# Kernel optimization log

Hardware: AMD Instinct MI355X
Metric: run time of the kernel (lower is better)

## Reference

```python
import jax, jax.numpy as jnp
import numpy as np

TEMPERATURE = 0.07
EPS = 1e-12  # matches torch F.normalize default eps


def setup_inputs() -> dict:
    key = jax.random.key(0)
    k1, k2 = jax.random.split(key)
    B, D = 8192, 256
    anchor = jax.random.normal(k1, (B, D), dtype=jnp.float32)
    positive = jax.random.normal(k2, (B, D), dtype=jnp.float32)
    return {"anchor": anchor, "positive": positive}


def _l2_normalize(x):
    # torch F.normalize(p=2, dim=1): x / max(||x||, eps)
    n = jnp.sqrt(jnp.sum(x * x, axis=1, keepdims=True))
    return x / jnp.maximum(n, EPS)


def reference(anchor, positive):
    a = _l2_normalize(anchor)
    p = _l2_normalize(positive)
    # normalized vectors -> cosine similarity is just a GEMM: (B, B)
    sim = jnp.einsum('id,jd->ij', a, p)
    B = sim.shape[0]
    # hard negative mining: max over off-diagonal entries per row
    neg = jnp.where(jnp.eye(B, dtype=bool), -jnp.inf, sim)
    max_neg = jnp.max(neg, axis=-1)  # (B,)
    logits = jnp.concatenate([sim, max_neg[:, None]], axis=1) / TEMPERATURE  # (B, B+1)
    labels = jnp.arange(B)
    logp = jax.nn.log_softmax(logits, axis=-1)
    loss = -jnp.mean(jnp.take_along_axis(logp, labels[:, None], axis=1))
    return loss
```

## Files before the change

### kernel.cpp

```cpp
#include <hip/hip_runtime.h>
#include <hip/hip_bf16.h>

using floatx4 = __attribute__((ext_vector_type(4))) float;
using int4v   = __attribute__((ext_vector_type(4))) int;
using int8v   = __attribute__((ext_vector_type(8))) int;

#define TEMP_INV 14.285714285714286f
#define DD 256
#define BM 128
#define NCT 8
#define SC1 127

typedef const __attribute__((address_space(1))) unsigned int* gptr_t;
typedef __attribute__((address_space(3))) unsigned int* lptr_t;

__device__ __forceinline__ void async_cp16(const void* g, void* l) {
  __builtin_amdgcn_global_load_lds((gptr_t)g, (lptr_t)l, 16, 0, 0);
}

__global__ __launch_bounds__(256) void nrm_kernel(
    const float* __restrict__ anchor, const float* __restrict__ positive,
    unsigned char* __restrict__ a8, unsigned char* __restrict__ p8,
    float* __restrict__ diag, float* __restrict__ out) {
  if (blockIdx.x == 0 && threadIdx.x == 0) out[0] = 0.f;
  const int wave = threadIdx.x >> 6;
  const int lane = threadIdx.x & 63;
  const int row  = blockIdx.x * 4 + wave;
  const float4 va = ((const float4*)(anchor   + (size_t)row * DD))[lane];
  const float4 vp = ((const float4*)(positive + (size_t)row * DD))[lane];
  float sa = va.x * va.x + va.y * va.y + va.z * va.z + va.w * va.w;
  float sp = vp.x * vp.x + vp.y * vp.y + vp.z * vp.z + vp.w * vp.w;
#pragma unroll
  for (int m = 32; m >= 1; m >>= 1) {
    sa += __shfl_xor(sa, m, 64);
    sp += __shfl_xor(sp, m, 64);
  }
  const float ka = 1.0f / fmaxf(sqrtf(sa), 1e-12f);
  const float kp = 1.0f / fmaxf(sqrtf(sp), 1e-12f);
  int pa = __builtin_amdgcn_cvt_pk_fp8_f32(va.x * ka, va.y * ka, 0, false);
  pa     = __builtin_amdgcn_cvt_pk_fp8_f32(va.z * ka, va.w * ka, pa, true);
  int pp = __builtin_amdgcn_cvt_pk_fp8_f32(vp.x * kp, vp.y * kp, 0, false);
  pp     = __builtin_amdgcn_cvt_pk_fp8_f32(vp.z * kp, vp.w * kp, pp, true);
  ((int*)(a8 + (size_t)row * DD))[lane] = pa;
  ((int*)(p8 + (size_t)row * DD))[lane] = pp;
  float d = __builtin_amdgcn_cvt_f32_fp8(pa, 0) * __builtin_amdgcn_cvt_f32_fp8(pp, 0)
          + __builtin_amdgcn_cvt_f32_fp8(pa, 1) * __builtin_amdgcn_cvt_f32_fp8(pp, 1)
          + __builtin_amdgcn_cvt_f32_fp8(pa, 2) * __builtin_amdgcn_cvt_f32_fp8(pp, 2)
          + __builtin_amdgcn_cvt_f32_fp8(pa, 3) * __builtin_amdgcn_cvt_f32_fp8(pp, 3);
#pragma unroll
  for (int m = 32; m >= 1; m >>= 1) d += __shfl_xor(d, m, 64);
  if (lane == 0) diag[row] = d;
}

__device__ __forceinline__ int8v fragLDS(const unsigned char* S, int row, int ks,
                                         int quad, int l16) {
  const int c0 = ks * 8 + quad * 2;
  const int4v lo = *(const int4v*)(S + row * DD + (((c0 + 0) ^ l16) << 4));
  const int4v hi = *(const int4v*)(S + row * DD + (((c0 + 1) ^ l16) << 4));
  return __builtin_shufflevector(lo, hi, 0, 1, 2, 3, 4, 5, 6, 7);
}

__device__ __forceinline__ int8v fragG(const unsigned char* g) {
  const int4v lo = *(const int4v*)(g);
  const int4v hi = *(const int4v*)(g + 16);
  return __builtin_shufflevector(lo, hi, 0, 1, 2, 3, 4, 5, 6, 7);
}

__global__ __launch_bounds__(512, 4) void gemm_stats(
    const unsigned char* __restrict__ a8, const unsigned char* __restrict__ p8,
    float* __restrict__ rsum, float* __restrict__ rmax, int Btot) {
  __shared__ __align__(16) unsigned char Bs[2][BM * DD];
  __shared__ float red_sum[2][BM];
  __shared__ float red_max[2][BM];

  const int t = threadIdx.x;
  const int wave = t >> 6, lane = t & 63;
  const int wm = wave & 3, wn = wave >> 2;
  const int quad = lane >> 4, l16 = lane & 15;
  const int row0    = blockIdx.y * BM;
  const int colbase = blockIdx.x * (NCT * BM);
  const bool hasdiag = ((int)(blockIdx.y >> 3) == (int)blockIdx.x);

  const int r4 = lane >> 4;
  const int cg = lane & 15;

  int8v a_frag[2][2];
  {
    const unsigned char* ab =
        a8 + (size_t)(row0 + wm * 32 + l16) * DD + quad * 32;
#pragma unroll
    for (int mi = 0; mi < 2; ++mi)
#pragma unroll
      for (int ks = 0; ks < 2; ++ks)
        a_frag[mi][ks] = fragG(ab + mi * 16 * DD + ks * 128);
  }

#pragma unroll
  for (int q = 0; q < 4; ++q) {
    const int rb = q * 32 + wave * 4;
    const int r  = rb + r4;
    async_cp16(p8 + (size_t)(colbase + r) * DD + (cg ^ (r & 15)) * 16,
               &Bs[0][rb * DD]);
  }

  float se_run[2][4], mx_run[2][4];
#pragma unroll
  for (int a = 0; a < 2; ++a)
#pragma unroll
    for (int b = 0; b < 4; ++b) { se_run[a][b] = 0.f; mx_run[a][b] = -INFINITY; }

  for (int ct = 0; ct < NCT; ++ct) {
    __syncthreads();

    if (ct + 1 < NCT) {
      const int colb = colbase + (ct + 1) * BM;
      unsigned char* dst = &Bs[(ct + 1) & 1][0];
#pragma unroll
      for (int q = 0; q < 4; ++q) {
        const int rb = q * 32 + wave * 4;
        const int r  = rb + r4;
        async_cp16(p8 + (size_t)(colb + r) * DD + (cg ^ (r & 15)) * 16,
                   dst + rb * DD);
      }
    }

    floatx4 acc[2][4];
#pragma unroll
    for (int a = 0; a < 2; ++a)
#pragma unroll
      for (int b = 0; b < 4; ++b) acc[a][b] = (floatx4){0.f, 0.f, 0.f, 0.f};

    const unsigned char* Bcur = &Bs[ct & 1][0];
#pragma unroll
    for (int ks = 0; ks < 2; ++ks) {
#pragma unroll
      for (int ni = 0; ni < 4; ++ni) {
        const int8v bf = fragLDS(Bcur, wn * 64 + ni * 16 + l16, ks, quad, l16);
        acc[0][ni] = __builtin_amdgcn_mfma_scale_f32_16x16x128_f8f6f4(
            a_frag[0][ks], bf, acc[0][ni], 0, 0, 0, SC1, 0, SC1);
        acc[1][ni] = __builtin_amdgcn_mfma_scale_f32_16x16x128_f8f6f4(
            a_frag[1][ks], bf, acc[1][ni], 0, 0, 0, SC1, 0, SC1);
      }
    }

    const int col0 = colbase + ct * BM;
    if (!hasdiag) {
#pragma unroll
      for (int mi = 0; mi < 2; ++mi)
#pragma unroll
        for (int reg = 0; reg < 4; ++reg)
#pragma unroll
          for (int ni = 0; ni < 4; ++ni) {
            const float s = acc[mi][ni][reg];
            se_run[mi][reg] += __expf(s * TEMP_INV);
            mx_run[mi][reg] = fmaxf(mx_run[mi][reg], s);
          }
    } else {
#pragma unroll
      for (int mi = 0; mi < 2; ++mi)
#pragma unroll
        for (int reg = 0; reg < 4; ++reg) {
          const int i = row0 + wm * 32 + mi * 16 + quad * 4 + reg;
#pragma unroll
          for (int ni = 0; ni < 4; ++ni) {
            const float s = acc[mi][ni][reg];
            const int j = col0 + wn * 64 + ni * 16 + l16;
            se_run[mi][reg] += __expf(s * TEMP_INV);
            mx_run[mi][reg] = fmaxf(mx_run[mi][reg], (i == j) ? -INFINITY : s);
          }
        }
    }
  }

#pragma unroll
  for (int mi = 0; mi < 2; ++mi) {
#pragma unroll
    for (int reg = 0; reg < 4; ++reg) {
      float se = se_run[mi][reg], mx = mx_run[mi][reg];
#pragma unroll
      for (int m = 1; m < 16; m <<= 1) {
        se += __shfl_xor(se, m, 64);
        mx = fmaxf(mx, __shfl_xor(mx, m, 64));
      }
      if (l16 == 0) {
        const int rb = wm * 32 + mi * 16 + quad * 4 + reg;
        red_sum[wn][rb] = se;
        red_max[wn][rb] = mx;
      }
    }
  }
  __syncthreads();
  if (t < BM) {
    rsum[(size_t)blockIdx.x * Btot + row0 + t] = red_sum[0][t] + red_sum[1][t];
    rmax[(size_t)blockIdx.x * Btot + row0 + t] = fmaxf(red_max[0][t], red_max[1][t]);
  }
}

__global__ __launch_bounds__(256) void row_loss_kernel(
    const float* __restrict__ rsum, const float* __restrict__ rmax,
    const float* __restrict__ diag, float* __restrict__ out, int Btot, int NG) {
  const int i = blockIdx.x * 256 + threadIdx.x;
  float s = 0.f, m = -INFINITY;
  for (int c = 0; c < NG; ++c) {
    s += rsum[(size_t)c * Btot + i];
    m = fmaxf(m, rmax[(size_t)c * Btot + i]);
  }
  float rl = __logf(s + __expf(m * TEMP_INV)) - diag[i] * TEMP_INV;
#pragma unroll
  for (int mm = 32; mm >= 1; mm >>= 1) rl += __shfl_xor(rl, mm, 64);
  __shared__ float red[4];
  if ((threadIdx.x & 63) == 0) red[threadIdx.x >> 6] = rl;
  __syncthreads();
  if (threadIdx.x == 0)
    atomicAdd(out, (red[0] + red[1] + red[2] + red[3]) / (float)Btot);
}

extern "C" void kernel_launch(void* const* d_in, const int* in_sizes, int n_in,
                              void* d_out, int out_size, void* d_ws, size_t ws_size,
                              hipStream_t stream) {
  const float* anchor   = (const float*)d_in[0];
  const float* positive = (const float*)d_in[1];
  const int B  = in_sizes[0] / DD;
  const int NG = B / (BM * NCT);
  const size_t BD = (size_t)B * DD;

  unsigned char* a8 = (unsigned char*)d_ws;
  unsigned char* p8 = a8 + BD;
  float* rsum  = (float*)(p8 + BD);
  float* rmax  = rsum + (size_t)NG * B;
  float* diag  = rmax + (size_t)NG * B;

  nrm_kernel<<<B / 4, 256, 0, stream>>>(anchor, positive, a8, p8, diag,
                                        (float*)d_out);
  dim3 g2(NG, B / BM);
  gemm_stats<<<g2, 512, 0, stream>>>(a8, p8, rsum, rmax, B);
  row_loss_kernel<<<B / 256, 256, 0, stream>>>(rsum, rmax, diag, (float*)d_out, B, NG);
}
```

Before: 108.4 us.

## Split column tile into two phases with barrier-synchronized MFMA and epilogue interleaving

Each column tile is now processed in two halves. Every half loads its LDS B fragments, issues half of the next tile's async global-to-LDS copies, hits a block barrier, then runs its MFMAs at raised wave priority followed by the exp/max epilogue. The aim is to spread memory traffic across the tile and to stagger the MFMA and exp work between waves, in a ping-pong style, so tensor and vector units overlap. The cost is extra s_barrier calls per tile and fixed sched_barrier points, which limit how freely the compiler can schedule instructions.

```diff
diff --git a/kernel.cpp b/kernel.cpp
--- a/kernel.cpp
+++ b/kernel.cpp
@@ -66,6 +66,11 @@
   return __builtin_shufflevector(lo, hi, 0, 1, 2, 3, 4, 5, 6, 7);
 }
 
+__device__ __forceinline__ floatx4 mfma_sc(int8v a, int8v b, floatx4 c) {
+  return __builtin_amdgcn_mfma_scale_f32_16x16x128_f8f6f4(a, b, c, 0, 0, 0,
+                                                          SC1, 0, SC1);
+}
+
 __global__ __launch_bounds__(512, 4) void gemm_stats(
     const unsigned char* __restrict__ a8, const unsigned char* __restrict__ p8,
     float* __restrict__ rsum, float* __restrict__ rmax, int Btot) {
@@ -112,63 +117,78 @@
   for (int ct = 0; ct < NCT; ++ct) {
     __syncthreads();
 
-    if (ct + 1 < NCT) {
-      const int colb = colbase + (ct + 1) * BM;
-      unsigned char* dst = &Bs[(ct + 1) & 1][0];
-#pragma unroll
-      for (int q = 0; q < 4; ++q) {
-        const int rb = q * 32 + wave * 4;
-        const int r  = rb + r4;
-        async_cp16(p8 + (size_t)(colb + r) * DD + (cg ^ (r & 15)) * 16,
-                   dst + rb * DD);
-      }
-    }
-
-    floatx4 acc[2][4];
-#pragma unroll
-    for (int a = 0; a < 2; ++a)
-#pragma unroll
-      for (int b = 0; b < 4; ++b) acc[a][b] = (floatx4){0.f, 0.f, 0.f, 0.f};
-
     const unsigned char* Bcur = &Bs[ct & 1][0];
-#pragma unroll
-    for (int ks = 0; ks < 2; ++ks) {
-#pragma unroll
-      for (int ni = 0; ni < 4; ++ni) {
-        const int8v bf = fragLDS(Bcur, wn * 64 + ni * 16 + l16, ks, quad, l16);
-        acc[0][ni] = __builtin_amdgcn_mfma_scale_f32_16x16x128_f8f6f4(
-            a_frag[0][ks], bf, acc[0][ni], 0, 0, 0, SC1, 0, SC1);
-        acc[1][ni] = __builtin_amdgcn_mfma_scale_f32_16x16x128_f8f6f4(
-            a_frag[1][ks], bf, acc[1][ni], 0, 0, 0, SC1, 0, SC1);
-      }
-    }
-
+    unsigned char* Bnxt = &Bs[(ct + 1) & 1][0];
+    const int colb = colbase + (ct + 1) * BM;
+    const bool dostage = (ct + 1 < NCT);
     const int col0 = colbase + ct * BM;
-    if (!hasdiag) {
-#pragma unroll
-      for (int mi = 0; mi < 2; ++mi)
-#pragma unroll
-        for (int reg = 0; reg < 4; ++reg)
-#pragma unroll
-          for (int ni = 0; ni < 4; ++ni) {
-            const float s = acc[mi][ni][reg];
-            se_run[mi][reg] += __expf(s * TEMP_INV);
-            mx_run[mi][reg] = fmaxf(mx_run[mi][reg], s);
+
+#pragma unroll
+    for (int p = 0; p < 2; ++p) {
+      const int nA = 2 * p, nB = 2 * p + 1;
+      const int8v bfA0 = fragLDS(Bcur, wn * 64 + nA * 16 + l16, 0, quad, l16);
+      const int8v bfA1 = fragLDS(Bcur, wn * 64 + nA * 16 + l16, 1, quad, l16);
+      const int8v bfB0 = fragLDS(Bcur, wn * 64 + nB * 16 + l16, 0, quad, l16);
+      const int8v bfB1 = fragLDS(Bcur, wn * 64 + nB * 16 + l16, 1, quad, l16);
+      if (dostage) {
+#pragma unroll
+        for (int q = 2 * p; q < 2 * p + 2; ++q) {
+          const int rb = q * 32 + wave * 4;
+          const int r  = rb + r4;
+          async_cp16(p8 + (size_t)(colb + r) * DD + (cg ^ (r & 15)) * 16,
+                     Bnxt + rb * DD);
+        }
+      }
+      __builtin_amdgcn_sched_barrier(0);
+      __builtin_amdgcn_s_barrier();
+      asm volatile("s_waitcnt lgkmcnt(0)" ::: "memory");
+      __builtin_amdgcn_sched_barrier(0);
+
+      floatx4 acc[2][2];
+#pragma unroll
+      for (int a = 0; a < 2; ++a)
+#pragma unroll
+        for (int b = 0; b < 2; ++b) acc[a][b] = (floatx4){0.f, 0.f, 0.f, 0.f};
+
+      __builtin_amdgcn_s_setprio(1);
+      acc[0][0] = mfma_sc(a_frag[0][0], bfA0, acc[0][0]);
+      acc[0][0] = mfma_sc(a_frag[0][1], bfA1, acc[0][0]);
+      acc[1][0] = mfma_sc(a_frag[1][0], bfA0, acc[1][0]);
+      acc[1][0] = mfma_sc(a_frag[1][1], bfA1, acc[1][0]);
+      acc[0][1] = mfma_sc(a_frag[0][0], bfB0, acc[0][1]);
+      acc[0][1] = mfma_sc(a_frag[0][1], bfB1, acc[0][1]);
+      acc[1][1] = mfma_sc(a_frag[1][0], bfB0, acc[1][1]);
+      acc[1][1] = mfma_sc(a_frag[1][1], bfB1, acc[1][1]);
+      __builtin_amdgcn_s_setprio(0);
+      __builtin_amdgcn_sched_barrier(0);
+      __builtin_amdgcn_s_barrier();
+
+      if (!hasdiag) {
+#pragma unroll
+        for (int mi = 0; mi < 2; ++mi)
+#pragma unroll
+          for (int reg = 0; reg < 4; ++reg)
+#pragma unroll
+            for (int h = 0; h < 2; ++h) {
+              const float s = acc[mi][h][reg];
+              se_run[mi][reg] += __expf(s * TEMP_INV);
+              mx_run[mi][reg] = fmaxf(mx_run[mi][reg], s);
+            }
+      } else {
+#pragma unroll
+        for (int mi = 0; mi < 2; ++mi)
+#pragma unroll
+          for (int reg = 0; reg < 4; ++reg) {
+            const int i = row0 + wm * 32 + mi * 16 + quad * 4 + reg;
+#pragma unroll
+            for (int h = 0; h < 2; ++h) {
+              const float s = acc[mi][h][reg];
+              const int j = col0 + wn * 64 + (2 * p + h) * 16 + l16;
+              se_run[mi][reg] += __expf(s * TEMP_INV);
+              mx_run[mi][reg] = fmaxf(mx_run[mi][reg], (i == j) ? -INFINITY : s);
+            }
           }
-    } else {
-#pragma unroll
-      for (int mi = 0; mi < 2; ++mi)
-#pragma unroll
-        for (int reg = 0; reg < 4; ++reg) {
-          const int i = row0 + wm * 32 + mi * 16 + quad * 4 + reg;
-#pragma unroll
-          for (int ni = 0; ni < 4; ++ni) {
-            const float s = acc[mi][ni][reg];
-            const int j = col0 + wn * 64 + ni * 16 + l16;
-            se_run[mi][reg] += __expf(s * TEMP_INV);
-            mx_run[mi][reg] = fmaxf(mx_run[mi][reg], (i == j) ? -INFINITY : s);
-          }
-        }
+      }
     }
   }
 
```

Measured after the change: 168.6 us. 1.56x slower.

## Use 256-thread blocks with single LDS buffer and split-half compute/epilogue overlap

Applied to the files above, without the earlier changes.

The GEMM-stats kernel now runs 4 waves per block, each wave covering 32 rows across the full 128-column tile, instead of 8 waves split 4x2. The double-buffered LDS tile becomes a single buffer. The next tile's async load is issued after the second half's MFMAs, so it overlaps the second half's exp/max epilogue. Per-block column groups are halved (NCT 4, giving twice as many grid column groups), and the cross-wave LDS reduction of row stats is dropped in favour of direct global writes. This cuts LDS use and barriers, at the cost of less prefetch distance and more partial rows for the final reduction kernel to combine.

```diff
diff --git a/kernel.cpp b/kernel.cpp
--- a/kernel.cpp
+++ b/kernel.cpp
@@ -7,8 +7,9 @@
 
 #define TEMP_INV 14.285714285714286f
 #define DD 256
-#define BM 128
-#define NCT 8
+#define BMR 128
+#define BNC 128
+#define NCT 4
 #define SC1 127
 
 typedef const __attribute__((address_space(1))) unsigned int* gptr_t;
@@ -66,28 +67,26 @@
   return __builtin_shufflevector(lo, hi, 0, 1, 2, 3, 4, 5, 6, 7);
 }
 
-__global__ __launch_bounds__(512, 4) void gemm_stats(
+__device__ __forceinline__ floatx4 mfma_sc(int8v a, int8v b, floatx4 c) {
+  return __builtin_amdgcn_mfma_scale_f32_16x16x128_f8f6f4(a, b, c, 0, 0, 0,
+                                                          SC1, 0, SC1);
+}
+
+__global__ __launch_bounds__(256, 4) void gemm_stats(
     const unsigned char* __restrict__ a8, const unsigned char* __restrict__ p8,
     float* __restrict__ rsum, float* __restrict__ rmax, int Btot) {
-  __shared__ __align__(16) unsigned char Bs[2][BM * DD];
-  __shared__ float red_sum[2][BM];
-  __shared__ float red_max[2][BM];
+  __shared__ __align__(16) unsigned char Bs[BNC * DD];
 
   const int t = threadIdx.x;
   const int wave = t >> 6, lane = t & 63;
-  const int wm = wave & 3, wn = wave >> 2;
   const int quad = lane >> 4, l16 = lane & 15;
-  const int row0    = blockIdx.y * BM;
-  const int colbase = blockIdx.x * (NCT * BM);
-  const bool hasdiag = ((int)(blockIdx.y >> 3) == (int)blockIdx.x);
-
-  const int r4 = lane >> 4;
-  const int cg = lane & 15;
+  const int row0    = blockIdx.y * BMR;
+  const int colbase = blockIdx.x * (NCT * BNC);
 
   int8v a_frag[2][2];
   {
     const unsigned char* ab =
-        a8 + (size_t)(row0 + wm * 32 + l16) * DD + quad * 32;
+        a8 + (size_t)(row0 + wave * 32 + l16) * DD + quad * 32;
 #pragma unroll
     for (int mi = 0; mi < 2; ++mi)
 #pragma unroll
@@ -96,11 +95,11 @@
   }
 
 #pragma unroll
-  for (int q = 0; q < 4; ++q) {
-    const int rb = q * 32 + wave * 4;
-    const int r  = rb + r4;
-    async_cp16(p8 + (size_t)(colbase + r) * DD + (cg ^ (r & 15)) * 16,
-               &Bs[0][rb * DD]);
+  for (int q = 0; q < 8; ++q) {
+    const int rb = q * 16 + wave * 4;
+    const int r  = rb + quad;
+    async_cp16(p8 + (size_t)(colbase + r) * DD + ((l16 ^ (r & 15)) << 4),
+               &Bs[rb * DD]);
   }
 
   float se_run[2][4], mx_run[2][4];
@@ -111,39 +110,77 @@
 
   for (int ct = 0; ct < NCT; ++ct) {
     __syncthreads();
-
+    const int col0 = colbase + ct * BNC;
+    const bool hasdiag = (blockIdx.y == blockIdx.x * NCT + ct);
+
+    floatx4 acc[2][4];
+#pragma unroll
+    for (int a = 0; a < 2; ++a)
+#pragma unroll
+      for (int b = 0; b < 4; ++b) acc[a][b] = (floatx4){0.f, 0.f, 0.f, 0.f};
+#pragma unroll
+    for (int ni = 0; ni < 4; ++ni) {
+      const int8v bf0 = fragLDS(Bs, ni * 16 + l16, 0, quad, l16);
+      const int8v bf1 = fragLDS(Bs, ni * 16 + l16, 1, quad, l16);
+      acc[0][ni] = mfma_sc(a_frag[0][0], bf0, acc[0][ni]);
+      acc[0][ni] = mfma_sc(a_frag[0][1], bf1, acc[0][ni]);
+      acc[1][ni] = mfma_sc(a_frag[1][0], bf0, acc[1][ni]);
+      acc[1][ni] = mfma_sc(a_frag[1][1], bf1, acc[1][ni]);
+    }
+    if (!hasdiag) {
+#pragma unroll
+      for (int mi = 0; mi < 2; ++mi)
+#pragma unroll
+        for (int reg = 0; reg < 4; ++reg)
+#pragma unroll
+          for (int ni = 0; ni < 4; ++ni) {
+            const float s = acc[mi][ni][reg];
+            se_run[mi][reg] += __expf(s * TEMP_INV);
+            mx_run[mi][reg] = fmaxf(mx_run[mi][reg], s);
+          }
+    } else {
+#pragma unroll
+      for (int mi = 0; mi < 2; ++mi)
+#pragma unroll
+        for (int reg = 0; reg < 4; ++reg) {
+          const int i = row0 + wave * 32 + mi * 16 + quad * 4 + reg;
+#pragma unroll
+          for (int ni = 0; ni < 4; ++ni) {
+            const float s = acc[mi][ni][reg];
+            const int j = col0 + ni * 16 + l16;
+            se_run[mi][reg] += __expf(s * TEMP_INV);
+            mx_run[mi][reg] = fmaxf(mx_run[mi][reg], (i == j) ? -INFINITY : s);
+          }
+        }
+    }
+
+    floatx4 acc2[2][4];
+#pragma unroll
+    for (int a = 0; a < 2; ++a)
+#pragma unroll
+      for (int b = 0; b < 4; ++b) acc2[a][b] = (floatx4){0.f, 0.f, 0.f, 0.f};
+#pragma unroll
+    for (int ni = 0; ni < 4; ++ni) {
+      const int8v bf0 = fragLDS(Bs, (ni + 4) * 16 + l16, 0, quad, l16);
+      const int8v bf1 = fragLDS(Bs, (ni + 4) * 16 + l16, 1, quad, l16);
+      acc2[0][ni] = mfma_sc(a_frag[0][0], bf0, acc2[0][ni]);
+      acc2[0][ni] = mfma_sc(a_frag[0][1], bf1, acc2[0][ni]);
+      acc2[1][ni] = mfma_sc(a_frag[1][0], bf0, acc2[1][ni]);
+      acc2[1][ni] = mfma_sc(a_frag[1][1], bf1, acc2[1][ni]);
+    }
+
+    __syncthreads();
     if (ct + 1 < NCT) {
-      const int colb = colbase + (ct + 1) * BM;
-      unsigned char* dst = &Bs[(ct + 1) & 1][0];
-#pragma unroll
-      for (int q = 0; q < 4; ++q) {
-        const int rb = q * 32 + wave * 4;
-        const int r  = rb + r4;
-        async_cp16(p8 + (size_t)(colb + r) * DD + (cg ^ (r & 15)) * 16,
-                   dst + rb * DD);
+      const int colb = colbase + (ct + 1) * BNC;
+#pragma unroll
+      for (int q = 0; q < 8; ++q) {
+        const int rb = q * 16 + wave * 4;
+        const int r  = rb + quad;
+        async_cp16(p8 + (size_t)(colb + r) * DD + ((l16 ^ (r & 15)) << 4),
+                   &Bs[rb * DD]);
       }
     }
 
-    floatx4 acc[2][4];
-#pragma unroll
-    for (int a = 0; a < 2; ++a)
-#pragma unroll
-      for (int b = 0; b < 4; ++b) acc[a][b] = (floatx4){0.f, 0.f, 0.f, 0.f};
-
-    const unsigned char* Bcur = &Bs[ct & 1][0];
-#pragma unroll
-    for (int ks = 0; ks < 2; ++ks) {
-#pragma unroll
-      for (int ni = 0; ni < 4; ++ni) {
-        const int8v bf = fragLDS(Bcur, wn * 64 + ni * 16 + l16, ks, quad, l16);
-        acc[0][ni] = __builtin_amdgcn_mfma_scale_f32_16x16x128_f8f6f4(
-            a_frag[0][ks], bf, acc[0][ni], 0, 0, 0, SC1, 0, SC1);
-        acc[1][ni] = __builtin_amdgcn_mfma_scale_f32_16x16x128_f8f6f4(
-            a_frag[1][ks], bf, acc[1][ni], 0, 0, 0, SC1, 0, SC1);
-      }
-    }
-
-    const int col0 = colbase + ct * BM;
     if (!hasdiag) {
 #pragma unroll
       for (int mi = 0; mi < 2; ++mi)
@@ -151,7 +188,7 @@
         for (int reg = 0; reg < 4; ++reg)
 #pragma unroll
           for (int ni = 0; ni < 4; ++ni) {
-            const float s = acc[mi][ni][reg];
+            const float s = acc2[mi][ni][reg];
             se_run[mi][reg] += __expf(s * TEMP_INV);
             mx_run[mi][reg] = fmaxf(mx_run[mi][reg], s);
           }
@@ -160,11 +197,11 @@
       for (int mi = 0; mi < 2; ++mi)
 #pragma unroll
         for (int reg = 0; reg < 4; ++reg) {
-          const int i = row0 + wm * 32 + mi * 16 + quad * 4 + reg;
-#pragma unroll
-          for (int ni = 0; ni < 4; ++ni) {
-            const float s = acc[mi][ni][reg];
-            const int j = col0 + wn * 64 + ni * 16 + l16;
+          const int i = row0 + wave * 32 + mi * 16 + quad * 4 + reg;
+#pragma unroll
+          for (int ni = 0; ni < 4; ++ni) {
+            const float s = acc2[mi][ni][reg];
+            const int j = col0 + (ni + 4) * 16 + l16;
             se_run[mi][reg] += __expf(s * TEMP_INV);
             mx_run[mi][reg] = fmaxf(mx_run[mi][reg], (i == j) ? -INFINITY : s);
           }
@@ -183,16 +220,11 @@
         mx = fmaxf(mx, __shfl_xor(mx, m, 64));
       }
       if (l16 == 0) {
-        const int rb = wm * 32 + mi * 16 + quad * 4 + reg;
-        red_sum[wn][rb] = se;
-        red_max[wn][rb] = mx;
+        const int r = wave * 32 + mi * 16 + quad * 4 + reg;
+        rsum[(size_t)blockIdx.x * Btot + row0 + r] = se;
+        rmax[(size_t)blockIdx.x * Btot + row0 + r] = mx;
       }
     }
-  }
-  __syncthreads();
-  if (t < BM) {
-    rsum[(size_t)blockIdx.x * Btot + row0 + t] = red_sum[0][t] + red_sum[1][t];
-    rmax[(size_t)blockIdx.x * Btot + row0 + t] = fmaxf(red_max[0][t], red_max[1][t]);
   }
 }
 
@@ -221,7 +253,7 @@
   const float* anchor   = (const float*)d_in[0];
   const float* positive = (const float*)d_in[1];
   const int B  = in_sizes[0] / DD;
-  const int NG = B / (BM * NCT);
+  const int NG = B / (BNC * NCT);
   const size_t BD = (size_t)B * DD;
 
   unsigned char* a8 = (unsigned char*)d_ws;
@@ -232,7 +264,7 @@
 
   nrm_kernel<<<B / 4, 256, 0, stream>>>(anchor, positive, a8, p8, diag,
                                         (float*)d_out);
-  dim3 g2(NG, B / BM);
-  gemm_stats<<<g2, 512, 0, stream>>>(a8, p8, rsum, rmax, B);
+  dim3 g2(NG, B / BMR);
+  gemm_stats<<<g2, 256, 0, stream>>>(a8, p8, rsum, rmax, B);
   row_loss_kernel<<<B / 256, 256, 0, stream>>>(rsum, rmax, diag, (float*)d_out, B, NG);
 }
```

Result: slower. 128.7 us (+18.8%).

## Store positive fp8 in fragment-major layout and load B fragments directly from global

Applied to the files above, without the earlier changes.

The normalization kernel now writes the fp8 positive matrix in a permuted layout matching the MFMA B-fragment order, so each lane's fragment is two contiguous-per-lane 16-byte loads. The GEMM kernel drops the LDS double buffer, async global-to-LDS copies and per-tile barriers, and loads B fragments straight from global memory (L2 cache). This removes LDS traffic and synchronization and frees shared memory for occupancy. In exchange, B reuse across the 4 M-waves now relies on cache hits instead of LDS, and the loads are no longer prefetched ahead of the MFMAs.

```diff
diff --git a/kernel.cpp b/kernel.cpp
--- a/kernel.cpp
+++ b/kernel.cpp
@@ -10,13 +10,6 @@
 #define BM 128
 #define NCT 8
 #define SC1 127
-
-typedef const __attribute__((address_space(1))) unsigned int* gptr_t;
-typedef __attribute__((address_space(3))) unsigned int* lptr_t;
-
-__device__ __forceinline__ void async_cp16(const void* g, void* l) {
-  __builtin_amdgcn_global_load_lds((gptr_t)g, (lptr_t)l, 16, 0, 0);
-}
 
 __global__ __launch_bounds__(256) void nrm_kernel(
     const float* __restrict__ anchor, const float* __restrict__ positive,
@@ -42,7 +35,16 @@
   int pp = __builtin_amdgcn_cvt_pk_fp8_f32(vp.x * kp, vp.y * kp, 0, false);
   pp     = __builtin_amdgcn_cvt_pk_fp8_f32(vp.z * kp, vp.w * kp, pp, true);
   ((int*)(a8 + (size_t)row * DD))[lane] = pa;
-  ((int*)(p8 + (size_t)row * DD))[lane] = pp;
+  {
+    const unsigned int off =
+        (unsigned)(row & ~15) * DD
+        + ((lane >> 5) << 11)
+        + (((lane >> 2) & 1) << 10)
+        + (((lane >> 3) & 3) << 8)
+        + ((row & 15) << 4)
+        + ((lane & 3) << 2);
+    *(int*)(p8 + off) = pp;
+  }
   float d = __builtin_amdgcn_cvt_f32_fp8(pa, 0) * __builtin_amdgcn_cvt_f32_fp8(pp, 0)
           + __builtin_amdgcn_cvt_f32_fp8(pa, 1) * __builtin_amdgcn_cvt_f32_fp8(pp, 1)
           + __builtin_amdgcn_cvt_f32_fp8(pa, 2) * __builtin_amdgcn_cvt_f32_fp8(pp, 2)
@@ -52,24 +54,20 @@
   if (lane == 0) diag[row] = d;
 }
 
-__device__ __forceinline__ int8v fragLDS(const unsigned char* S, int row, int ks,
-                                         int quad, int l16) {
-  const int c0 = ks * 8 + quad * 2;
-  const int4v lo = *(const int4v*)(S + row * DD + (((c0 + 0) ^ l16) << 4));
-  const int4v hi = *(const int4v*)(S + row * DD + (((c0 + 1) ^ l16) << 4));
-  return __builtin_shufflevector(lo, hi, 0, 1, 2, 3, 4, 5, 6, 7);
-}
-
 __device__ __forceinline__ int8v fragG(const unsigned char* g) {
   const int4v lo = *(const int4v*)(g);
   const int4v hi = *(const int4v*)(g + 16);
   return __builtin_shufflevector(lo, hi, 0, 1, 2, 3, 4, 5, 6, 7);
 }
 
+__device__ __forceinline__ floatx4 mfma_sc(int8v a, int8v b, floatx4 c) {
+  return __builtin_amdgcn_mfma_scale_f32_16x16x128_f8f6f4(a, b, c, 0, 0, 0,
+                                                          SC1, 0, SC1);
+}
+
 __global__ __launch_bounds__(512, 4) void gemm_stats(
     const unsigned char* __restrict__ a8, const unsigned char* __restrict__ p8,
     float* __restrict__ rsum, float* __restrict__ rmax, int Btot) {
-  __shared__ __align__(16) unsigned char Bs[2][BM * DD];
   __shared__ float red_sum[2][BM];
   __shared__ float red_max[2][BM];
 
@@ -81,9 +79,6 @@
   const int colbase = blockIdx.x * (NCT * BM);
   const bool hasdiag = ((int)(blockIdx.y >> 3) == (int)blockIdx.x);
 
-  const int r4 = lane >> 4;
-  const int cg = lane & 15;
-
   int8v a_frag[2][2];
   {
     const unsigned char* ab =
@@ -95,14 +90,6 @@
         a_frag[mi][ks] = fragG(ab + mi * 16 * DD + ks * 128);
   }
 
-#pragma unroll
-  for (int q = 0; q < 4; ++q) {
-    const int rb = q * 32 + wave * 4;
-    const int r  = rb + r4;
-    async_cp16(p8 + (size_t)(colbase + r) * DD + (cg ^ (r & 15)) * 16,
-               &Bs[0][rb * DD]);
-  }
-
   float se_run[2][4], mx_run[2][4];
 #pragma unroll
   for (int a = 0; a < 2; ++a)
@@ -110,40 +97,28 @@
     for (int b = 0; b < 4; ++b) { se_run[a][b] = 0.f; mx_run[a][b] = -INFINITY; }
 
   for (int ct = 0; ct < NCT; ++ct) {
-    __syncthreads();
-
-    if (ct + 1 < NCT) {
-      const int colb = colbase + (ct + 1) * BM;
-      unsigned char* dst = &Bs[(ct + 1) & 1][0];
-#pragma unroll
-      for (int q = 0; q < 4; ++q) {
-        const int rb = q * 32 + wave * 4;
-        const int r  = rb + r4;
-        async_cp16(p8 + (size_t)(colb + r) * DD + (cg ^ (r & 15)) * 16,
-                   dst + rb * DD);
+    const int col0 = colbase + ct * BM;
+    const unsigned char* bb = p8 + (size_t)(col0 + wn * 64) * DD + lane * 16;
+
+    floatx4 acc[2][4];
+#pragma unroll
+    for (int a = 0; a < 2; ++a)
+#pragma unroll
+      for (int b = 0; b < 4; ++b) acc[a][b] = (floatx4){0.f, 0.f, 0.f, 0.f};
+
+#pragma unroll
+    for (int ks = 0; ks < 2; ++ks) {
+#pragma unroll
+      for (int ni = 0; ni < 4; ++ni) {
+        const unsigned char* c = bb + ni * 4096 + ks * 2048;
+        const int4v lo = *(const int4v*)(c);
+        const int4v hi = *(const int4v*)(c + 1024);
+        const int8v bf = __builtin_shufflevector(lo, hi, 0, 1, 2, 3, 4, 5, 6, 7);
+        acc[0][ni] = mfma_sc(a_frag[0][ks], bf, acc[0][ni]);
+        acc[1][ni] = mfma_sc(a_frag[1][ks], bf, acc[1][ni]);
       }
     }
 
-    floatx4 acc[2][4];
-#pragma unroll
-    for (int a = 0; a < 2; ++a)
-#pragma unroll
-      for (int b = 0; b < 4; ++b) acc[a][b] = (floatx4){0.f, 0.f, 0.f, 0.f};
-
-    const unsigned char* Bcur = &Bs[ct & 1][0];
-#pragma unroll
-    for (int ks = 0; ks < 2; ++ks) {
-#pragma unroll
-      for (int ni = 0; ni < 4; ++ni) {
-        const int8v bf = fragLDS(Bcur, wn * 64 + ni * 16 + l16, ks, quad, l16);
-        acc[0][ni] = __builtin_amdgcn_mfma_scale_f32_16x16x128_f8f6f4(
-            a_frag[0][ks], bf, acc[0][ni], 0, 0, 0, SC1, 0, SC1);
-        acc[1][ni] = __builtin_amdgcn_mfma_scale_f32_16x16x128_f8f6f4(
-            a_frag[1][ks], bf, acc[1][ni], 0, 0, 0, SC1, 0, SC1);
-      }
-    }
-
-    const int col0 = colbase + ct * BM;
     if (!hasdiag) {
 #pragma unroll
       for (int mi = 0; mi < 2; ++mi)
```

Result: no change. 110.0 us (+1.5%).
